# Kernel optimization log

Measured on AMD Instinct MI355X. Metric: run time of the kernel, lower is better.

## Reference

```python
import jax, jax.numpy as jnp
import numpy as np

D_MODEL = 512
NUM_HEADS = 8
HEAD_DIM = D_MODEL // NUM_HEADS


def setup_inputs() -> dict:
    key = jax.random.key(0)
    ks = jax.random.split(key, 11)
    N, S, D = 2, 4096, D_MODEL
    s = 1.0 / np.sqrt(D)
    return {
        "query": jax.random.normal(ks[0], (N, S, D), jnp.float32),
        "key": jax.random.normal(ks[1], (N, S, D), jnp.float32),
        "value": jax.random.normal(ks[2], (N, S, D), jnp.float32),
        "Wq": jax.random.normal(ks[3], (D, D), jnp.float32) * s,
        "bq": jnp.zeros((D,), jnp.float32),
        "Wk": jax.random.normal(ks[4], (D, D), jnp.float32) * s,
        "bk": jnp.zeros((D,), jnp.float32),
        "Wv": jax.random.normal(ks[5], (D, D), jnp.float32) * s,
        "bv": jnp.zeros((D,), jnp.float32),
        "Wo": jax.random.normal(ks[6], (D, D), jnp.float32) * s,
        "bo": jnp.zeros((D,), jnp.float32),
    }


def reference(query, key, value, Wq, bq, Wk, bk, Wv, bv, Wo, bo):
    N, S, D = query.shape
    H, Hd = NUM_HEADS, HEAD_DIM
    # Linear projections (torch Linear: x @ W.T + b), split heads -> [N,H,S,Hd]
    Q = (query @ Wq.T + bq).reshape(N, S, H, Hd).transpose(0, 2, 1, 3)
    K = (key @ Wk.T + bk).reshape(N, S, H, Hd).transpose(0, 2, 1, 3)
    V = (value @ Wv.T + bv).reshape(N, S, H, Hd).transpose(0, 2, 1, 3)
    scale = 1.0 / np.sqrt(Hd)
    energy = jnp.einsum("nhqd,nhkd->nhqk", Q, K) * scale  # [N,H,S,S]
    attention = jax.nn.softmax(energy, axis=-1)
    out = jnp.einsum("nhqk,nhkd->nhqd", attention, V)
    out = out.transpose(0, 2, 1, 3).reshape(N, S, D)
    return out @ Wo.T + bo
```

## Files before the change

### kernel.cpp

```cpp
#include <hip/hip_runtime.h>


#define SEQ 4096
#define PERHEAD 262144
#define CEXPF 0.18033688011112042f

typedef short bf16x8 __attribute__((ext_vector_type(8)));
typedef short bf16x4 __attribute__((ext_vector_type(4)));
typedef float f32x4 __attribute__((ext_vector_type(4)));
typedef unsigned short u16;
typedef unsigned int u32;

__device__ inline float bf2f(u16 h) {
    return __uint_as_float(((u32)h) << 16);
}
__device__ inline u16 f2bf(float f) {
    u32 u = __float_as_uint(f);
    u = (u + 0x7fffu + ((u >> 16) & 1u)) >> 16;
    return (u16)u;
}
__device__ inline u32 packtrunc(float lo, float hi) {
    return __builtin_amdgcn_perm(__float_as_uint(hi), __float_as_uint(lo),
                                 0x07060302u);
}
__device__ inline uint4 pack8(float4 a, float4 b) {
    uint4 r;
    r.x = (u32)f2bf(a.x) | ((u32)f2bf(a.y) << 16);
    r.y = (u32)f2bf(a.z) | ((u32)f2bf(a.w) << 16);
    r.z = (u32)f2bf(b.x) | ((u32)f2bf(b.y) << 16);
    r.w = (u32)f2bf(b.z) | ((u32)f2bf(b.w) << 16);
    return r;
}

__global__ void detect_dtype(const u16* __restrict__ W, int* __restrict__ flag) {
    const int lane = threadIdx.x & 63;
    u16 u = W[2 * lane];
    int e = (u >> 7) & 0xFF;
    int plaus = (u == 0) || (e >= 100 && e <= 132);
    unsigned long long m = __ballot(plaus);
    if (lane == 0) *flag = (__popcll(m) >= 48) ? 0 : 1;
}

__global__ __launch_bounds__(256) void prep(
    const void* __restrict__ W0, const void* __restrict__ W1,
    const void* __restrict__ W2, const void* __restrict__ W3,
    const void* __restrict__ b0, const void* __restrict__ b1,
    const void* __restrict__ b2, const void* __restrict__ b3,
    u16* __restrict__ Wc, u16* __restrict__ bc, const int* __restrict__ flag)
{
    const int m = blockIdx.y;
    const void* Ws = (m == 0) ? W0 : (m == 1) ? W1 : (m == 2) ? W2 : W3;
    const void* bs = (m == 0) ? b0 : (m == 1) ? b1 : (m == 2) ? b2 : b3;
    const int isf32 = *flag;
    if (blockIdx.x < 128) {
        const int idx = blockIdx.x * 2048 + threadIdx.x * 8;
        u16* dst = Wc + (size_t)m * 262144 + idx;
        if (isf32) {
            const float4* s = (const float4*)((const float*)Ws + idx);
            *(uint4*)dst = pack8(s[0], s[1]);
        } else {
            *(uint4*)dst = *(const uint4*)((const u16*)Ws + idx);
        }
    } else if (threadIdx.x < 64) {
        const int idx = threadIdx.x * 8;
        u16* dst = bc + m * 512 + idx;
        if (isf32) {
            const float4* s = (const float4*)((const float*)bs + idx);
            *(uint4*)dst = pack8(s[0], s[1]);
        } else {
            *(uint4*)dst = *(const uint4*)((const u16*)bs + idx);
        }
    }
}

template <int A_BF16>
__device__ inline void gemm_body(
    const void* __restrict__ Av, const u16* __restrict__ B,
    const u16* __restrict__ bias, void* __restrict__ outv,
    int isf32, int mode, float scale, int m0, int n0,
    u16* As, u16* Bs)
{
    const int tid = threadIdx.x;
    const int wave = tid >> 6, lane = tid & 63, quad = lane >> 4, ln = lane & 15;
    const int qr = wave >> 1, qc = wave & 1;

    f32x4 acc[4][4];
#pragma unroll
    for (int i = 0; i < 4; i++)
#pragma unroll
        for (int j = 0; j < 4; j++) acc[i][j] = (f32x4){0.f, 0.f, 0.f, 0.f};

    const int srow = tid >> 1;
    const int scol = (tid & 1) * 16;
    const uint4*  Ag16 = (const uint4*) ((const u16*)Av + (size_t)(m0 + srow) * 512 + scol);
    const float4* Ag32 = (const float4*)((const float*)Av + (size_t)(m0 + srow) * 512 + scol);
    const uint4*  Bg   = (const uint4*) (B + (size_t)(n0 + srow) * 512 + scol);
    uint4* Al = (uint4*)(As + srow * 40 + scol);
    uint4* Bl = (uint4*)(Bs + srow * 40 + scol);

    for (int kk = 0; kk < 512; kk += 32) {
        __syncthreads();
        uint4 aw0, aw1;
        if (A_BF16 || !isf32) {
            aw0 = Ag16[0]; aw1 = Ag16[1];
            Ag16 += 4;
        } else {
            float4 f0 = Ag32[0], f1 = Ag32[1], f2 = Ag32[2], f3 = Ag32[3];
            Ag32 += 8;
            aw0 = pack8(f0, f1); aw1 = pack8(f2, f3);
        }
        uint4 bw0 = Bg[0], bw1 = Bg[1];
        Bg += 4;
        Al[0] = aw0; Al[1] = aw1; Bl[0] = bw0; Bl[1] = bw1;
        __syncthreads();
        bf16x8 af[4], bfr[4];
#pragma unroll
        for (int mi = 0; mi < 4; mi++)
            af[mi] = *(const bf16x8*)(As + (qr * 64 + mi * 16 + ln) * 40 + quad * 8);
#pragma unroll
        for (int ni = 0; ni < 4; ni++)
            bfr[ni] = *(const bf16x8*)(Bs + (qc * 64 + ni * 16 + ln) * 40 + quad * 8);
#pragma unroll
        for (int mi = 0; mi < 4; mi++)
#pragma unroll
            for (int ni = 0; ni < 4; ni++)
                acc[mi][ni] = __builtin_amdgcn_mfma_f32_16x16x32_bf16(
                    af[mi], bfr[ni], acc[mi][ni], 0, 0, 0);
    }

#pragma unroll
    for (int ni = 0; ni < 4; ni++) {
        const int col = n0 + qc * 64 + ni * 16 + ln;
        const float bvv = bf2f(bias[col]);
#pragma unroll
        for (int mi = 0; mi < 4; mi++) {
#pragma unroll
            for (int r = 0; r < 4; r++) {
                const int row = m0 + qr * 64 + mi * 16 + quad * 4 + r;
                const float v = (acc[mi][ni][r] + bvv) * scale;
                if (mode == 0) {
                    const size_t idx = (size_t)row * 512 + col;
                    if (isf32) ((float*)outv)[idx] = v;
                    else       ((u16*)outv)[idx] = f2bf(v);
                } else {
                    const int b = row >> 12, s = row & 4095;
                    const int h = col >> 6, hd = col & 63;
                    size_t idx;
                    if (mode == 1) {
                        idx = (size_t)(b * 8 + h) * PERHEAD + (size_t)s * 64 + hd;
                    } else {
                        const int s6 = s & 63;
                        const int p = (s6 & 32) | ((s6 & 12) << 1) |
                                      ((s6 & 16) >> 2) | (s6 & 3);
                        idx = (size_t)(b * 8 + h) * PERHEAD + (size_t)hd * 4096 +
                              (size_t)((s & ~63) + p);
                    }
                    ((u16*)outv)[idx] = f2bf(v);
                }
            }
        }
    }
}

__global__ __launch_bounds__(256) void qkv_proj(
    const void* __restrict__ q, const void* __restrict__ k, const void* __restrict__ v,
    const u16* __restrict__ Wc, const u16* __restrict__ bc,
    u16* __restrict__ Qh, u16* __restrict__ Kh, u16* __restrict__ Vt,
    const int* __restrict__ flag)
{
    __shared__ __align__(16) u16 As[128 * 40];
    __shared__ __align__(16) u16 Bs[128 * 40];
    const int z = blockIdx.z;
    const void* Av = (z == 0) ? q : (z == 1) ? k : v;
    void* outv = (z == 0) ? (void*)Qh : (z == 1) ? (void*)Kh : (void*)Vt;
    const int mode = (z == 2) ? 2 : 1;
    const float scale = (z == 0) ? CEXPF : 1.0f;
    gemm_body<0>(Av, Wc + (size_t)z * 262144, bc + z * 512, outv,
                 *flag, mode, scale, blockIdx.y * 128, blockIdx.x * 128, As, Bs);
}

__global__ __launch_bounds__(256) void out_proj(
    const void* __restrict__ Av, const u16* __restrict__ Wc,
    const u16* __restrict__ bc, void* __restrict__ outv,
    const int* __restrict__ flag)
{
    __shared__ __align__(16) u16 As[128 * 40];
    __shared__ __align__(16) u16 Bs[128 * 40];
    gemm_body<1>(Av, Wc + (size_t)3 * 262144, bc + 3 * 512, outv,
                 *flag, 0, 1.0f, blockIdx.y * 128, blockIdx.x * 128, As, Bs);
}

__global__ __launch_bounds__(512) void attn_kernel(
    const u16* __restrict__ Q, const u16* __restrict__ K,
    const u16* __restrict__ Vt, u16* __restrict__ AO)
{
    __shared__ __align__(16) u16 S[2][2][2][64 * 72];

    const int tid = threadIdx.x;
    const int g = tid >> 8;
    const int wq = (tid >> 6) & 3;
    const int lane = tid & 63, quad = lane >> 4, ln = lane & 15;
    const int bh = blockIdx.y;
    const int q0 = blockIdx.x * 128;
    const size_t base = (size_t)bh * PERHEAD;

    bf16x8 qf[2][2];
#pragma unroll
    for (int qt = 0; qt < 2; qt++) {
        const uint4* qp = (const uint4*)(Q + base + (size_t)(q0 + wq * 32 + qt * 16 + ln) * 64);
        uint4 v0 = qp[quad], v1 = qp[4 + quad];
        qf[qt][0] = *(bf16x8*)&v0;
        qf[qt][1] = *(bf16x8*)&v1;
    }

    bf16x8 ones;
#pragma unroll
    for (int j = 0; j < 8; j++) ones[j] = (short)0x3F80;

    f32x4 oT[2][4];
    f32x4 lacc[2];
#pragma unroll
    for (int qt = 0; qt < 2; qt++) {
        lacc[qt] = (f32x4){0.f, 0.f, 0.f, 0.f};
#pragma unroll
        for (int mt = 0; mt < 4; mt++) oT[qt][mt] = (f32x4){0.f, 0.f, 0.f, 0.f};
    }

    const int tid2 = tid & 255;
    const int srow = tid2 >> 2;
    const int sc = (tid2 & 3) * 16;
    const uint4* Kg = (const uint4*)(K + base + (size_t)(g * 2048 + srow) * 64 + sc);
    const uint4* Vg = (const uint4*)(Vt + base + (size_t)srow * 4096 + g * 2048 + sc);
    const int soff = srow * 72 + sc;

    {
        uint4 a = Kg[0], b = Kg[1], c = Vg[0], d = Vg[1];
        Kg += 512; Vg += 8;
        uint4* Kl = (uint4*)(&S[g][0][0][0] + soff);
        uint4* Vl = (uint4*)(&S[g][0][1][0] + soff);
        Kl[0] = a; Kl[1] = b; Vl[0] = c; Vl[1] = d;
    }
    __syncthreads();

    for (int it = 0; it < 32; ++it) {
        const u16* Kc = &S[g][it & 1][0][0];
        const u16* Vc = &S[g][it & 1][1][0];

        uint4 pa = Kg[0], pb = Kg[1], pc = Vg[0], pd = Vg[1];
        Kg += 512; Vg += 8;

        f32x4 s[2][4];
        __builtin_amdgcn_s_setprio(1);
#pragma unroll
        for (int t = 0; t < 2; t++)
#pragma unroll
            for (int kt = 0; kt < 4; kt++) {
                bf16x8 kf = *(const bf16x8*)(Kc + (kt * 16 + ln) * 72 + t * 32 + quad * 8);
#pragma unroll
                for (int qt = 0; qt < 2; qt++) {
                    if (t == 0)
                        s[qt][kt] = __builtin_amdgcn_mfma_f32_16x16x32_bf16(
                            kf, qf[qt][0], (f32x4){0.f, 0.f, 0.f, 0.f}, 0, 0, 0);
                    else
                        s[qt][kt] = __builtin_amdgcn_mfma_f32_16x16x32_bf16(
                            kf, qf[qt][1], s[qt][kt], 0, 0, 0);
                }
            }
        __builtin_amdgcn_s_setprio(0);

        bf16x8 pf[2][2];
#pragma unroll
        for (int qt = 0; qt < 2; qt++)
#pragma unroll
            for (int c = 0; c < 2; c++) {
                float e0 = __builtin_amdgcn_exp2f(s[qt][2 * c][0]);
                float e1 = __builtin_amdgcn_exp2f(s[qt][2 * c][1]);
                float e2 = __builtin_amdgcn_exp2f(s[qt][2 * c][2]);
                float e3 = __builtin_amdgcn_exp2f(s[qt][2 * c][3]);
                float f0 = __builtin_amdgcn_exp2f(s[qt][2 * c + 1][0]);
                float f1 = __builtin_amdgcn_exp2f(s[qt][2 * c + 1][1]);
                float f2 = __builtin_amdgcn_exp2f(s[qt][2 * c + 1][2]);
                float f3 = __builtin_amdgcn_exp2f(s[qt][2 * c + 1][3]);
                u32 w0 = packtrunc(e0, e1), w1 = packtrunc(e2, e3);
                u32 w2 = packtrunc(f0, f1), w3 = packtrunc(f2, f3);
                uint4 pk = {w0, w1, w2, w3};
                pf[qt][c] = *(bf16x8*)&pk;
            }

        __builtin_amdgcn_s_setprio(1);
#pragma unroll
        for (int qt = 0; qt < 2; qt++)
#pragma unroll
            for (int c = 0; c < 2; c++)
                lacc[qt] = __builtin_amdgcn_mfma_f32_16x16x32_bf16(
                    ones, pf[qt][c], lacc[qt], 0, 0, 0);

#pragma unroll
        for (int c = 0; c < 2; c++)
#pragma unroll
            for (int mt = 0; mt < 4; mt++) {
                bf16x8 vf = *(const bf16x8*)(Vc + (mt * 16 + ln) * 72 + c * 32 + quad * 8);
#pragma unroll
                for (int qt = 0; qt < 2; qt++)
                    oT[qt][mt] = __builtin_amdgcn_mfma_f32_16x16x32_bf16(
                        vf, pf[qt][c], oT[qt][mt], 0, 0, 0);
            }
        __builtin_amdgcn_s_setprio(0);

        {
            uint4* Kl = (uint4*)(&S[g][(it + 1) & 1][0][0] + soff);
            uint4* Vl = (uint4*)(&S[g][(it + 1) & 1][1][0] + soff);
            Kl[0] = pa; Kl[1] = pb; Vl[0] = pc; Vl[1] = pd;
        }
        __syncthreads();
    }

    float* Xch = (float*)&S[0][0][0][0];
    if (g == 1) {
#pragma unroll
        for (int qt = 0; qt < 2; qt++) {
#pragma unroll
            for (int mt = 0; mt < 4; mt++)
#pragma unroll
                for (int r = 0; r < 4; r++)
                    Xch[(((wq * 2 + qt) * 4 + mt) * 16 + quad * 4 + r) * 17 + ln] =
                        oT[qt][mt][r];
            if (quad == 0)
                Xch[8704 + (wq * 2 + qt) * 16 + ln] = lacc[qt][0];
        }
    }
    __syncthreads();
    if (g == 0) {
        const int b = bh >> 3, h = bh & 7;
#pragma unroll
        for (int qt = 0; qt < 2; qt++) {
            const float l2 = Xch[8704 + (wq * 2 + qt) * 16 + ln];
            const float inv = 1.0f / (lacc[qt][0] + l2);
            const int qrow = q0 + wq * 32 + qt * 16 + ln;
            u16* op = AO + (size_t)(b * 4096 + qrow) * 512 + h * 64 + quad * 4;
#pragma unroll
            for (int mt = 0; mt < 4; mt++) {
                float o0 = oT[qt][mt][0] +
                    Xch[(((wq * 2 + qt) * 4 + mt) * 16 + quad * 4 + 0) * 17 + ln];
                float o1 = oT[qt][mt][1] +
                    Xch[(((wq * 2 + qt) * 4 + mt) * 16 + quad * 4 + 1) * 17 + ln];
                float o2 = oT[qt][mt][2] +
                    Xch[(((wq * 2 + qt) * 4 + mt) * 16 + quad * 4 + 2) * 17 + ln];
                float o3 = oT[qt][mt][3] +
                    Xch[(((wq * 2 + qt) * 4 + mt) * 16 + quad * 4 + 3) * 17 + ln];
                uint2 pk;
                pk.x = (u32)f2bf(o0 * inv) | ((u32)f2bf(o1 * inv) << 16);
                pk.y = (u32)f2bf(o2 * inv) | ((u32)f2bf(o3 * inv) << 16);
                *(uint2*)(op + mt * 16) = pk;
            }
        }
    }
}

extern "C" void kernel_launch(void* const* d_in, const int* in_sizes, int n_in,
                              void* d_out, int out_size, void* d_ws, size_t ws_size,
                              hipStream_t stream)
{
    (void)in_sizes; (void)n_in; (void)out_size; (void)ws_size;
    const void* q  = d_in[0];
    const void* k  = d_in[1];
    const void* v  = d_in[2];
    const void* Wq = d_in[3];
    const void* bq = d_in[4];
    const void* Wk = d_in[5];
    const void* bk = d_in[6];
    const void* Wv = d_in[7];
    const void* bv = d_in[8];
    const void* Wo = d_in[9];
    const void* bo = d_in[10];

    u16* ws = (u16*)d_ws;
    u16* Kh = ws;
    u16* Vt = ws + 4194304;
    u16* AO = ws + 8388608;
    u16* Wc = ws + 12582912;
    u16* bc = ws + 12582912 + 1048576;
    int* flag = (int*)(ws + 12582912 + 1048576 + 2048);
    u16* Qh = (u16*)d_out;

    detect_dtype<<<1, 64, 0, stream>>>((const u16*)Wq, flag);
    prep<<<dim3(129, 4), 256, 0, stream>>>(Wq, Wk, Wv, Wo, bq, bk, bv, bo,
                                           Wc, bc, flag);
    qkv_proj<<<dim3(4, 64, 3), 256, 0, stream>>>(q, k, v, Wc, bc, Qh, Kh, Vt, flag);
    attn_kernel<<<dim3(32, 16), 512, 0, stream>>>(Qh, Kh, Vt, AO);
    out_proj<<<dim3(4, 64), 256, 0, stream>>>(AO, Wc, bc, d_out, flag);
}
```

Baseline: 242.0 us.

## Halve GEMM N-tile and attention key tile to shrink LDS and add blocks

The projection GEMMs now use 128x64 output tiles instead of 128x128, which doubles the grid and halves B-tile shared memory and accumulator registers. The attention kernel processes 32 keys per iteration instead of 64 (64 iterations), with a repacked shared-memory layout that is roughly half the previous size. The aim is higher occupancy and more blocks in flight across the CUs. The cost is more loop iterations and barriers per block, and less data reuse per tile in the GEMMs.

Measured after the change: 263.3 us. +8.8%, slower.

```diff
diff --git a/kernel.cpp b/kernel.cpp
--- a/kernel.cpp
+++ b/kernel.cpp
@@ -73,30 +73,33 @@
     }
 }
 
-template <int A_BF16>
+template <int A_BF16, int NT>
 __device__ inline void gemm_body(
     const void* __restrict__ Av, const u16* __restrict__ B,
     const u16* __restrict__ bias, void* __restrict__ outv,
     int isf32, int mode, float scale, int m0, int n0,
     u16* As, u16* Bs)
 {
+    constexpr int NI = NT / 32;
     const int tid = threadIdx.x;
     const int wave = tid >> 6, lane = tid & 63, quad = lane >> 4, ln = lane & 15;
     const int qr = wave >> 1, qc = wave & 1;
 
-    f32x4 acc[4][4];
+    f32x4 acc[4][NI];
 #pragma unroll
     for (int i = 0; i < 4; i++)
 #pragma unroll
-        for (int j = 0; j < 4; j++) acc[i][j] = (f32x4){0.f, 0.f, 0.f, 0.f};
+        for (int j = 0; j < NI; j++) acc[i][j] = (f32x4){0.f, 0.f, 0.f, 0.f};
 
     const int srow = tid >> 1;
     const int scol = (tid & 1) * 16;
     const uint4*  Ag16 = (const uint4*) ((const u16*)Av + (size_t)(m0 + srow) * 512 + scol);
     const float4* Ag32 = (const float4*)((const float*)Av + (size_t)(m0 + srow) * 512 + scol);
-    const uint4*  Bg   = (const uint4*) (B + (size_t)(n0 + srow) * 512 + scol);
+    const int brow = (NT == 128) ? (tid >> 1) : (tid >> 2);
+    const int bcol = (NT == 128) ? ((tid & 1) * 16) : ((tid & 3) * 8);
+    const uint4*  Bg = (const uint4*)(B + (size_t)(n0 + brow) * 512 + bcol);
     uint4* Al = (uint4*)(As + srow * 40 + scol);
-    uint4* Bl = (uint4*)(Bs + srow * 40 + scol);
+    uint4* Bl = (uint4*)(Bs + brow * 40 + bcol);
 
     for (int kk = 0; kk < 512; kk += 32) {
         __syncthreads();
@@ -109,28 +112,31 @@
             Ag32 += 8;
             aw0 = pack8(f0, f1); aw1 = pack8(f2, f3);
         }
-        uint4 bw0 = Bg[0], bw1 = Bg[1];
+        uint4 bw0 = Bg[0], bw1 = {};
+        if (NT == 128) bw1 = Bg[1];
         Bg += 4;
-        Al[0] = aw0; Al[1] = aw1; Bl[0] = bw0; Bl[1] = bw1;
+        Al[0] = aw0; Al[1] = aw1;
+        Bl[0] = bw0;
+        if (NT == 128) Bl[1] = bw1;
         __syncthreads();
-        bf16x8 af[4], bfr[4];
+        bf16x8 af[4], bfr[NI];
 #pragma unroll
         for (int mi = 0; mi < 4; mi++)
             af[mi] = *(const bf16x8*)(As + (qr * 64 + mi * 16 + ln) * 40 + quad * 8);
 #pragma unroll
-        for (int ni = 0; ni < 4; ni++)
-            bfr[ni] = *(const bf16x8*)(Bs + (qc * 64 + ni * 16 + ln) * 40 + quad * 8);
+        for (int ni = 0; ni < NI; ni++)
+            bfr[ni] = *(const bf16x8*)(Bs + (qc * (NT / 2) + ni * 16 + ln) * 40 + quad * 8);
 #pragma unroll
         for (int mi = 0; mi < 4; mi++)
 #pragma unroll
-            for (int ni = 0; ni < 4; ni++)
+            for (int ni = 0; ni < NI; ni++)
                 acc[mi][ni] = __builtin_amdgcn_mfma_f32_16x16x32_bf16(
                     af[mi], bfr[ni], acc[mi][ni], 0, 0, 0);
     }
 
 #pragma unroll
-    for (int ni = 0; ni < 4; ni++) {
-        const int col = n0 + qc * 64 + ni * 16 + ln;
+    for (int ni = 0; ni < NI; ni++) {
+        const int col = n0 + qc * (NT / 2) + ni * 16 + ln;
         const float bvv = bf2f(bias[col]);
 #pragma unroll
         for (int mi = 0; mi < 4; mi++) {
@@ -169,14 +175,14 @@
     const int* __restrict__ flag)
 {
     __shared__ __align__(16) u16 As[128 * 40];
-    __shared__ __align__(16) u16 Bs[128 * 40];
+    __shared__ __align__(16) u16 Bs[64 * 40];
     const int z = blockIdx.z;
     const void* Av = (z == 0) ? q : (z == 1) ? k : v;
     void* outv = (z == 0) ? (void*)Qh : (z == 1) ? (void*)Kh : (void*)Vt;
     const int mode = (z == 2) ? 2 : 1;
     const float scale = (z == 0) ? CEXPF : 1.0f;
-    gemm_body<0>(Av, Wc + (size_t)z * 262144, bc + z * 512, outv,
-                 *flag, mode, scale, blockIdx.y * 128, blockIdx.x * 128, As, Bs);
+    gemm_body<0, 64>(Av, Wc + (size_t)z * 262144, bc + z * 512, outv,
+                     *flag, mode, scale, blockIdx.y * 128, blockIdx.x * 64, As, Bs);
 }
 
 __global__ __launch_bounds__(256) void out_proj(
@@ -185,16 +191,16 @@
     const int* __restrict__ flag)
 {
     __shared__ __align__(16) u16 As[128 * 40];
-    __shared__ __align__(16) u16 Bs[128 * 40];
-    gemm_body<1>(Av, Wc + (size_t)3 * 262144, bc + 3 * 512, outv,
-                 *flag, 0, 1.0f, blockIdx.y * 128, blockIdx.x * 128, As, Bs);
+    __shared__ __align__(16) u16 Bs[64 * 40];
+    gemm_body<1, 64>(Av, Wc + (size_t)3 * 262144, bc + 3 * 512, outv,
+                     *flag, 0, 1.0f, blockIdx.y * 128, blockIdx.x * 64, As, Bs);
 }
 
 __global__ __launch_bounds__(512) void attn_kernel(
     const u16* __restrict__ Q, const u16* __restrict__ K,
     const u16* __restrict__ Vt, u16* __restrict__ AO)
 {
-    __shared__ __align__(16) u16 S[2][2][2][64 * 72];
+    __shared__ __align__(16) u16 SM[19456];
 
     const int tid = threadIdx.x;
     const int g = tid >> 8;
@@ -227,34 +233,34 @@
     }
 
     const int tid2 = tid & 255;
-    const int srow = tid2 >> 2;
-    const int sc = (tid2 & 3) * 16;
-    const uint4* Kg = (const uint4*)(K + base + (size_t)(g * 2048 + srow) * 64 + sc);
-    const uint4* Vg = (const uint4*)(Vt + base + (size_t)srow * 4096 + g * 2048 + sc);
-    const int soff = srow * 72 + sc;
+    const int srowK = tid2 >> 3, scK = (tid2 & 7) * 8;
+    const int srowV = tid2 >> 2, scV = (tid2 & 3) * 8;
+    const uint4* Kg = (const uint4*)(K + base + (size_t)(g * 2048 + srowK) * 64 + scK);
+    const uint4* Vg = (const uint4*)(Vt + base + (size_t)srowV * 4096 + g * 2048 + scV);
+    const int kloff = srowK * 72 + scK;
+    const int vloff = srowV * 40 + scV;
 
     {
-        uint4 a = Kg[0], b = Kg[1], c = Vg[0], d = Vg[1];
-        Kg += 512; Vg += 8;
-        uint4* Kl = (uint4*)(&S[g][0][0][0] + soff);
-        uint4* Vl = (uint4*)(&S[g][0][1][0] + soff);
-        Kl[0] = a; Kl[1] = b; Vl[0] = c; Vl[1] = d;
+        uint4 a = Kg[0], c = Vg[0];
+        Kg += 256; Vg += 4;
+        *(uint4*)(SM + (g * 2 + 0) * 2304 + kloff) = a;
+        *(uint4*)(SM + 9216 + (g * 2 + 0) * 2560 + vloff) = c;
     }
     __syncthreads();
 
-    for (int it = 0; it < 32; ++it) {
-        const u16* Kc = &S[g][it & 1][0][0];
-        const u16* Vc = &S[g][it & 1][1][0];
-
-        uint4 pa = Kg[0], pb = Kg[1], pc = Vg[0], pd = Vg[1];
-        Kg += 512; Vg += 8;
-
-        f32x4 s[2][4];
+    for (int it = 0; it < 64; ++it) {
+        const u16* Kc = SM + (g * 2 + (it & 1)) * 2304;
+        const u16* Vc = SM + 9216 + (g * 2 + (it & 1)) * 2560;
+
+        uint4 pa = Kg[0], pc = Vg[0];
+        Kg += 256; Vg += 4;
+
+        f32x4 s[2][2];
         __builtin_amdgcn_s_setprio(1);
 #pragma unroll
         for (int t = 0; t < 2; t++)
 #pragma unroll
-            for (int kt = 0; kt < 4; kt++) {
+            for (int kt = 0; kt < 2; kt++) {
                 bf16x8 kf = *(const bf16x8*)(Kc + (kt * 16 + ln) * 72 + t * 32 + quad * 8);
 #pragma unroll
                 for (int qt = 0; qt < 2; qt++) {
@@ -268,54 +274,45 @@
             }
         __builtin_amdgcn_s_setprio(0);
 
-        bf16x8 pf[2][2];
+        bf16x8 pf[2];
+#pragma unroll
+        for (int qt = 0; qt < 2; qt++) {
+            float e0 = __builtin_amdgcn_exp2f(s[qt][0][0]);
+            float e1 = __builtin_amdgcn_exp2f(s[qt][0][1]);
+            float e2 = __builtin_amdgcn_exp2f(s[qt][0][2]);
+            float e3 = __builtin_amdgcn_exp2f(s[qt][0][3]);
+            float f0 = __builtin_amdgcn_exp2f(s[qt][1][0]);
+            float f1 = __builtin_amdgcn_exp2f(s[qt][1][1]);
+            float f2 = __builtin_amdgcn_exp2f(s[qt][1][2]);
+            float f3 = __builtin_amdgcn_exp2f(s[qt][1][3]);
+            u32 w0 = packtrunc(e0, e1), w1 = packtrunc(e2, e3);
+            u32 w2 = packtrunc(f0, f1), w3 = packtrunc(f2, f3);
+            uint4 pk = {w0, w1, w2, w3};
+            pf[qt] = *(bf16x8*)&pk;
+        }
+
+        __builtin_amdgcn_s_setprio(1);
 #pragma unroll
         for (int qt = 0; qt < 2; qt++)
-#pragma unroll
-            for (int c = 0; c < 2; c++) {
-                float e0 = __builtin_amdgcn_exp2f(s[qt][2 * c][0]);
-                float e1 = __builtin_amdgcn_exp2f(s[qt][2 * c][1]);
-                float e2 = __builtin_amdgcn_exp2f(s[qt][2 * c][2]);
-                float e3 = __builtin_amdgcn_exp2f(s[qt][2 * c][3]);
-                float f0 = __builtin_amdgcn_exp2f(s[qt][2 * c + 1][0]);
-                float f1 = __builtin_amdgcn_exp2f(s[qt][2 * c + 1][1]);
-                float f2 = __builtin_amdgcn_exp2f(s[qt][2 * c + 1][2]);
-                float f3 = __builtin_amdgcn_exp2f(s[qt][2 * c + 1][3]);
-                u32 w0 = packtrunc(e0, e1), w1 = packtrunc(e2, e3);
-                u32 w2 = packtrunc(f0, f1), w3 = packtrunc(f2, f3);
-                uint4 pk = {w0, w1, w2, w3};
-                pf[qt][c] = *(bf16x8*)&pk;
-            }
-
-        __builtin_amdgcn_s_setprio(1);
-#pragma unroll
-        for (int qt = 0; qt < 2; qt++)
-#pragma unroll
-            for (int c = 0; c < 2; c++)
-                lacc[qt] = __builtin_amdgcn_mfma_f32_16x16x32_bf16(
-                    ones, pf[qt][c], lacc[qt], 0, 0, 0);
-
-#pragma unroll
-        for (int c = 0; c < 2; c++)
-#pragma unroll
-            for (int mt = 0; mt < 4; mt++) {
-                bf16x8 vf = *(const bf16x8*)(Vc + (mt * 16 + ln) * 72 + c * 32 + quad * 8);
-#pragma unroll
-                for (int qt = 0; qt < 2; qt++)
-                    oT[qt][mt] = __builtin_amdgcn_mfma_f32_16x16x32_bf16(
-                        vf, pf[qt][c], oT[qt][mt], 0, 0, 0);
-            }
+            lacc[qt] = __builtin_amdgcn_mfma_f32_16x16x32_bf16(
+                ones, pf[qt], lacc[qt], 0, 0, 0);
+
+#pragma unroll
+        for (int mt = 0; mt < 4; mt++) {
+            bf16x8 vf = *(const bf16x8*)(Vc + (mt * 16 + ln) * 40 + quad * 8);
+#pragma unroll
+            for (int qt = 0; qt < 2; qt++)
+                oT[qt][mt] = __builtin_amdgcn_mfma_f32_16x16x32_bf16(
+                    vf, pf[qt], oT[qt][mt], 0, 0, 0);
+        }
         __builtin_amdgcn_s_setprio(0);
 
-        {
-            uint4* Kl = (uint4*)(&S[g][(it + 1) & 1][0][0] + soff);
-            uint4* Vl = (uint4*)(&S[g][(it + 1) & 1][1][0] + soff);
-            Kl[0] = pa; Kl[1] = pb; Vl[0] = pc; Vl[1] = pd;
-        }
+        *(uint4*)(SM + (g * 2 + ((it + 1) & 1)) * 2304 + kloff) = pa;
+        *(uint4*)(SM + 9216 + (g * 2 + ((it + 1) & 1)) * 2560 + vloff) = pc;
         __syncthreads();
     }
 
-    float* Xch = (float*)&S[0][0][0][0];
+    float* Xch = (float*)SM;
     if (g == 1) {
 #pragma unroll
         for (int qt = 0; qt < 2; qt++) {
@@ -386,7 +383,7 @@
     detect_dtype<<<1, 64, 0, stream>>>((const u16*)Wq, flag);
     prep<<<dim3(129, 4), 256, 0, stream>>>(Wq, Wk, Wv, Wo, bq, bk, bv, bo,
                                            Wc, bc, flag);
-    qkv_proj<<<dim3(4, 64, 3), 256, 0, stream>>>(q, k, v, Wc, bc, Qh, Kh, Vt, flag);
+    qkv_proj<<<dim3(8, 64, 3), 256, 0, stream>>>(q, k, v, Wc, bc, Qh, Kh, Vt, flag);
     attn_kernel<<<dim3(32, 16), 512, 0, stream>>>(Qh, Kh, Vt, AO);
-    out_proj<<<dim3(4, 64), 256, 0, stream>>>(AO, Wc, bc, d_out, flag);
-}
+    out_proj<<<dim3(8, 64), 256, 0, stream>>>(AO, Wc, bc, d_out, flag);
+}
```
